# Performance work log

Measured on AMD Instinct MI355X. Metric: run time of the kernel, lower is better.

## Reference

```python
import jax, jax.numpy as jnp
import numpy as np


def _conv(x, w, b, stride, pad):
    y = jax.lax.conv_general_dilated(
        x, w, window_strides=(stride, stride),
        padding=((pad, pad), (pad, pad)),
        dimension_numbers=('NCHW', 'OIHW', 'NCHW'))
    return y + b[None, :, None, None]


def setup_inputs() -> dict:
    key = jax.random.key(0)
    ks = jax.random.split(key, 10)
    B, C, H, W = 4, 3, 256, 256
    HID, D, K = 128, 32, 65536
    s = 0.05
    return {
        'x': jax.random.normal(ks[0], (B, C, H, W), dtype=jnp.float32),
        'w1': jax.random.normal(ks[1], (HID, C, 4, 4), dtype=jnp.float32) * s,
        'b1': jnp.zeros((HID,), dtype=jnp.float32),
        'w2': jax.random.normal(ks[2], (HID, HID, 4, 4), dtype=jnp.float32) * s,
        'b2': jnp.zeros((HID,), dtype=jnp.float32),
        'w3': jax.random.normal(ks[3], (HID, HID, 4, 4), dtype=jnp.float32) * s,
        'b3': jnp.zeros((HID,), dtype=jnp.float32),
        'w4': jax.random.normal(ks[4], (D, HID, 3, 3), dtype=jnp.float32) * s,
        'b4': jnp.zeros((D,), dtype=jnp.float32),
        'codebook': jax.random.normal(ks[5], (K, D), dtype=jnp.float32),
    }


def reference(x, w1, b1, w2, b2, w3, b3, w4, b4, codebook):
    z = jax.nn.relu(_conv(x, w1, b1, 2, 1))
    z = jax.nn.relu(_conv(z, w2, b2, 2, 1))
    z = jax.nn.relu(_conv(z, w3, b3, 2, 1))
    z = _conv(z, w4, b4, 1, 1)                 # [B, D, h, w]
    z = jnp.transpose(z, (0, 2, 3, 1))          # [B, h, w, D]
    B, h, w, D = z.shape
    zf = z.reshape(-1, D)                        # [N, D]
    # pairwise squared distances: ||z||^2 + ||e||^2 - 2 z.e
    d = (jnp.sum(zf * zf, axis=1, keepdims=True)
         + jnp.sum(codebook * codebook, axis=1)[None, :]
         - 2.0 * jnp.matmul(zf, codebook.T))    # [N, K]
    idx = jnp.argmin(d, axis=1)                  # [N]
    z_q = codebook[idx].reshape(B, h, w, D)
    return idx.reshape(B, h, w), z_q
```

## Files before the change

### kernel.cpp

```cpp
#include <hip/hip_runtime.h>
#include <cfloat>

typedef float f32x4 __attribute__((ext_vector_type(4)));
typedef _Float16 h8 __attribute__((ext_vector_type(8)));

static __device__ __forceinline__ unsigned umin_(unsigned a, unsigned b) { return a < b ? a : b; }
static __device__ __forceinline__ unsigned umax_(unsigned a, unsigned b) { return a > b ? a : b; }
static __device__ __forceinline__ unsigned med3_(unsigned a, unsigned b, unsigned c) {
    unsigned d;
    asm("v_med3_u32 %0, %1, %2, %3" : "=v"(d) : "v"(a), "v"(b), "v"(c));
    return d;
}

static __device__ __forceinline__ void gl_lds16(const h8* g, h8* s) {
    __builtin_amdgcn_global_load_lds(
        (const __attribute__((address_space(1))) unsigned int*)g,
        (__attribute__((address_space(3))) unsigned int*)s, 16, 0, 0);
}

__global__ __launch_bounds__(256)
void prep_k(_Float16* p0, _Float16* p1, _Float16* p2, _Float16* p3,
            _Float16* p4, _Float16* p5,
            const float* __restrict__ w2, const float* __restrict__ w3,
            const float* __restrict__ w4,
            h8* __restrict__ B2h, h8* __restrict__ B2l,
            h8* __restrict__ B3h, h8* __restrict__ B3l,
            h8* __restrict__ B4h, h8* __restrict__ B4l) {
    const int bx = blockIdx.x;
    const int tid = threadIdx.x;

    if (bx < 96) {
        const int s = bx >> 4, plane = bx & 15;
        _Float16* p; int np, P;
        switch (s) {
            case 0: p = p0; np = 16; P = 66; break;
            case 1: p = p1; np = 16; P = 66; break;
            case 2: p = p2; np = 16; P = 34; break;
            case 3: p = p3; np = 16; P = 34; break;
            case 4: p = p4; np = 4;  P = 34; break;
            default: p = p5; np = 4; P = 34; break;
        }
        if (plane >= np) return;
        _Float16* pl = p + (size_t)plane * P * P * 128;
        const int rowN = P * 128;
        for (int i = tid; i < rowN; i += 256) {
            pl[i] = (_Float16)0.f;
            pl[(size_t)(P - 1) * rowN + i] = (_Float16)0.f;
            const int r = i >> 7, c = i & 127;
            pl[(size_t)r * rowN + c] = (_Float16)0.f;
            pl[(size_t)r * rowN + (P - 1) * 128 + c] = (_Float16)0.f;
        }
    } else {
        const int layer = (bx - 96) >> 7;
        const int bxx = (bx - 96) & 127;
        const float* w; h8 *Bh, *Bl; int T, NT, KHKW;
        switch (layer) {
            case 0:  w = w2; Bh = B2h; Bl = B2l; T = 16; NT = 8; KHKW = 16; break;
            case 1:  w = w3; Bh = B3h; Bl = B3l; T = 16; NT = 8; KHKW = 16; break;
            default: w = w4; Bh = B4h; Bl = B4l; T = 9;  NT = 2; KHKW = 9;  break;
        }
        const int idx = bxx * 256 + tid;
        if (idx >= T * 4 * NT * 64) return;
        const int lane = idx & 63;
        int r = idx >> 6;
        const int nt = r % NT; r /= NT;
        const int ks = r & 3;  r >>= 2;
        const int t = r;
        const int oc = nt * 16 + (lane & 15);
        const int icb = ks * 32 + (lane >> 4) * 8;
        h8 hv, lv;
#pragma unroll
        for (int j = 0; j < 8; ++j) {
            const float v = w[(size_t)(oc * 128 + icb + j) * KHKW + t];
            _Float16 h = (_Float16)v;
            hv[j] = h;
            lv[j] = (_Float16)((v - (float)h) * 2048.f);
        }
        Bh[idx] = hv;
        Bl[idx] = lv;
    }
}

__global__ __launch_bounds__(256)
void conv1_k(const float* __restrict__ in, const float* __restrict__ w,
             const float* __restrict__ bias,
             _Float16* __restrict__ Dh, _Float16* __restrict__ Dl) {
    __shared__ float tile[3][34 * 36];
    const int tid = threadIdx.x;
    const int tx = tid & 15, ty = tid >> 4;
    const int bx = blockIdx.x & 7, by = blockIdx.x >> 3;
    const int oc0 = blockIdx.y * 8;
    const int b = blockIdx.z;
    const int ox = bx * 16 + tx, oy = by * 16 + ty;
    const int ix0 = bx * 32 - 1, iy0 = by * 32 - 1;

    for (int f = tid; f < 3 * 34 * 34; f += 256) {
        const int ic = f / 1156, r2 = f % 1156;
        const int r = r2 / 34, c = r2 % 34;
        const int iy = iy0 + r, ix = ix0 + c;
        float v = ((unsigned)iy < 256u && (unsigned)ix < 256u)
                      ? in[((size_t)(b * 3 + ic) * 256 + iy) * 256 + ix] : 0.f;
        tile[ic][r * 36 + c] = v;
    }
    __syncthreads();

    float acc[8];
#pragma unroll
    for (int j = 0; j < 8; ++j) acc[j] = 0.f;
#pragma unroll
    for (int ic = 0; ic < 3; ++ic) {
#pragma unroll
        for (int kh = 0; kh < 4; ++kh) {
            const float2* p = (const float2*)&tile[ic][(2 * ty + kh) * 36 + 2 * tx];
            const float2 r0 = p[0], r1 = p[1];
            const float tap[4] = {r0.x, r0.y, r1.x, r1.y};
#pragma unroll
            for (int kw = 0; kw < 4; ++kw)
#pragma unroll
                for (int j = 0; j < 8; ++j)
                    acc[j] = fmaf(tap[kw], w[((oc0 + j) * 3 + ic) * 16 + kh * 4 + kw], acc[j]);
        }
    }

    h8 hv, lv;
#pragma unroll
    for (int j = 0; j < 8; ++j) {
        float r = fmaxf(acc[j] + bias[oc0 + j], 0.f);
        _Float16 h = (_Float16)r;
        hv[j] = h;
        lv[j] = (_Float16)((r - (float)h) * 2048.f);
    }
    const size_t di = (((size_t)((b * 2 + (oy & 1)) * 2 + (ox & 1)) * 66 + 1 + (oy >> 1)) * 66
                       + 1 + (ox >> 1)) * 128 + oc0;
    *(h8*)(Dh + di) = hv;
    *(h8*)(Dl + di) = lv;
}

template<int WN, int MT, bool SPLIT>
__global__ __launch_bounds__(256, 1)
void gemmS2_k(const _Float16* __restrict__ Ah, const _Float16* __restrict__ Al,
              const h8* __restrict__ Bh, const h8* __restrict__ Bl,
              const float* __restrict__ bias,
              _Float16* __restrict__ Dh, _Float16* __restrict__ Dl,
              int OW, int OH, int PP, int dPP) {
    constexpr int NW_N = 8 / WN;
    constexpr int NW_M = 4 / NW_N;
    __shared__ h8 lH[2][2048];
    __shared__ h8 lL[2][2048];

    const int tid = threadIdx.x, wid = tid >> 6, l = tid & 63;
    const int nq = wid % NW_N, mi = wid / NW_N;
    const int mt0 = (blockIdx.x * NW_M + mi) * MT;
    const int mpr = OW >> 4, mpi = OH * mpr;
    const int laneA = (l & 15) * 128 + (l >> 4) * 8;

    int bm[MT], oym[MT], oxm[MT];
#pragma unroll
    for (int m = 0; m < MT; ++m) {
        const int mt = mt0 + m;
        bm[m] = mt / mpi;
        const int rem = mt % mpi;
        oym[m] = rem / mpr;
        oxm[m] = (rem % mpr) << 4;
    }

    f32x4 a1[MT][WN], am[MT][WN];
#pragma unroll
    for (int m = 0; m < MT; ++m)
#pragma unroll
        for (int s = 0; s < WN; ++s) {
            a1[m][s] = (f32x4){0.f, 0.f, 0.f, 0.f};
            am[m][s] = (f32x4){0.f, 0.f, 0.f, 0.f};
        }

    {
        const h8* sh = Bh + wid * 512 + l;
        const h8* sl = Bl + wid * 512 + l;
#pragma unroll
        for (int i = 0; i < 8; ++i) gl_lds16(sh + i * 64, &lH[0][wid * 512 + i * 64]);
#pragma unroll
        for (int i = 0; i < 8; ++i) gl_lds16(sl + i * 64, &lL[0][wid * 512 + i * 64]);
    }
    __syncthreads();

#pragma unroll 1
    for (int t = 0; t < 16; ++t) {
        const int cur = t & 1;
        const int kh = t >> 2, kw = t & 3;
        const int dy = (kh - 1) >> 1, dx = (kw - 1) >> 1;
        const int py = (kh - 1) & 1, px = (kw - 1) & 1;
        h8 avh[MT][4], avl[MT][4];
#pragma unroll
        for (int m = 0; m < MT; ++m) {
            const int pidx = (bm[m] * 2 + py) * 2 + px;
            const size_t abase = ((size_t)(pidx * PP + (oym[m] + dy + 1)) * PP
                                  + (oxm[m] + dx + 1)) * 128 + laneA;
#pragma unroll
            for (int ks = 0; ks < 4; ++ks) {
                avh[m][ks] = *(const h8*)(Ah + abase + ks * 32);
                avl[m][ks] = *(const h8*)(Al + abase + ks * 32);
            }
        }
        if (t + 1 < 16) {
            const int nxt = cur ^ 1;
            const h8* sh = Bh + (size_t)(t + 1) * 2048 + wid * 512 + l;
            const h8* sl = Bl + (size_t)(t + 1) * 2048 + wid * 512 + l;
#pragma unroll
            for (int i = 0; i < 8; ++i) gl_lds16(sh + i * 64, &lH[nxt][wid * 512 + i * 64]);
#pragma unroll
            for (int i = 0; i < 8; ++i) gl_lds16(sl + i * 64, &lL[nxt][wid * 512 + i * 64]);
        }
#pragma unroll
        for (int ks = 0; ks < 4; ++ks) {
#pragma unroll
            for (int s = 0; s < WN; ++s) {
                const h8 bvh = lH[cur][(ks * 8 + nq * WN + s) * 64 + l];
                const h8 bvl = lL[cur][(ks * 8 + nq * WN + s) * 64 + l];
#pragma unroll
                for (int m = 0; m < MT; ++m) {
                    a1[m][s] = __builtin_amdgcn_mfma_f32_16x16x32_f16(avh[m][ks], bvh, a1[m][s], 0, 0, 0);
                    am[m][s] = __builtin_amdgcn_mfma_f32_16x16x32_f16(avh[m][ks], bvl, am[m][s], 0, 0, 0);
                    am[m][s] = __builtin_amdgcn_mfma_f32_16x16x32_f16(avl[m][ks], bvh, am[m][s], 0, 0, 0);
                }
            }
        }
        __syncthreads();
    }

#pragma unroll
    for (int m = 0; m < MT; ++m) {
#pragma unroll
        for (int s = 0; s < WN; ++s) {
            const int oc = (nq * WN + s) * 16 + (l & 15);
            const float bv = bias[oc];
#pragma unroll
            for (int i = 0; i < 4; ++i) {
                const int row = (l >> 4) * 4 + i;
                float v = fmaf(am[m][s][i], 4.8828125e-4f, a1[m][s][i]);
                v = fmaxf(v + bv, 0.f);
                _Float16 h = (_Float16)v;
                _Float16 lo = (_Float16)((v - (float)h) * 2048.f);
                const int oxp = oxm[m] + row;
                const int oy = oym[m], b = bm[m];
                size_t di;
                if constexpr (SPLIT) {
                    di = (((size_t)((b * 2 + (oy & 1)) * 2 + (oxp & 1)) * dPP
                           + 1 + (oy >> 1)) * dPP + 1 + (oxp >> 1)) * 128 + oc;
                } else {
                    di = ((size_t)(b * dPP + 1 + oy) * dPP + 1 + oxp) * 128 + oc;
                }
                Dh[di] = h;
                Dl[di] = lo;
            }
        }
    }
}

template<int S, bool FIN, int WPN, int MT>
__global__ __launch_bounds__(256)
void gemm_k(const _Float16* __restrict__ Ah, const _Float16* __restrict__ Al,
            const h8* __restrict__ Bh, const h8* __restrict__ Bl,
            float* __restrict__ part, const float* __restrict__ bias,
            _Float16* __restrict__ Dh, _Float16* __restrict__ Dl,
            int OW, int OH, int PP, int NT, int TPS, int M, int N, int dPP) {
    const int tid = threadIdx.x, wid = tid >> 6, l = tid & 63;
    const int ntb = wid % WPN;
    const int mt0 = (blockIdx.x * (4 / WPN) + wid / WPN) * MT;
    const int sp = blockIdx.y;
    const int mpr = OW >> 4, mpi = OH * mpr;
    const int laneA = (l & 15) * 128 + (l >> 4) * 8;

    int bmt[MT], oymt[MT], oxmt[MT];
#pragma unroll
    for (int m = 0; m < MT; ++m) {
        const int mt = mt0 + m;
        bmt[m] = mt / mpi;
        const int rem = mt % mpi;
        oymt[m] = rem / mpr;
        oxmt[m] = (rem % mpr) << 4;
    }

    f32x4 a1[MT][2], am[MT][2];
#pragma unroll
    for (int m = 0; m < MT; ++m)
#pragma unroll
        for (int s = 0; s < 2; ++s) {
            a1[m][s] = (f32x4){0.f, 0.f, 0.f, 0.f};
            am[m][s] = (f32x4){0.f, 0.f, 0.f, 0.f};
        }

    const int t0 = sp * TPS, t1 = t0 + TPS;
#pragma unroll 2
    for (int t = t0; t < t1; ++t) {
        int dy, dx, pidx[MT];
        if constexpr (S == 2) {
            const int kh = t >> 2, kw = t & 3;
            dy = (kh - 1) >> 1; dx = (kw - 1) >> 1;
            const int py = (kh - 1) & 1, px = (kw - 1) & 1;
#pragma unroll
            for (int m = 0; m < MT; ++m) pidx[m] = (bmt[m] * 2 + py) * 2 + px;
        } else {
            dy = t / 3 - 1; dx = t % 3 - 1;
#pragma unroll
            for (int m = 0; m < MT; ++m) pidx[m] = bmt[m];
        }
        const _Float16* pAh[MT]; const _Float16* pAl[MT];
#pragma unroll
        for (int m = 0; m < MT; ++m) {
            const size_t base = ((size_t)(pidx[m] * PP + (oymt[m] + dy + 1)) * PP
                                 + (oxmt[m] + dx + 1)) * 128 + laneA;
            pAh[m] = Ah + base;
            pAl[m] = Al + base;
        }
        const size_t bbase = ((size_t)(t * 4) * NT + ntb * 2) * 64 + l;
#pragma unroll
        for (int ks = 0; ks < 4; ++ks) {
            h8 avh[MT], avl[MT];
#pragma unroll
            for (int m = 0; m < MT; ++m) {
                avh[m] = *(const h8*)(pAh[m] + ks * 32);
                avl[m] = *(const h8*)(pAl[m] + ks * 32);
            }
#pragma unroll
            for (int s = 0; s < 2; ++s) {
                const h8 bvh = Bh[bbase + (size_t)ks * NT * 64 + s * 64];
                const h8 bvl = Bl[bbase + (size_t)ks * NT * 64 + s * 64];
#pragma unroll
                for (int m = 0; m < MT; ++m) {
                    a1[m][s] = __builtin_amdgcn_mfma_f32_16x16x32_f16(avh[m], bvh, a1[m][s], 0, 0, 0);
                    am[m][s] = __builtin_amdgcn_mfma_f32_16x16x32_f16(avh[m], bvl, am[m][s], 0, 0, 0);
                    am[m][s] = __builtin_amdgcn_mfma_f32_16x16x32_f16(avl[m], bvh, am[m][s], 0, 0, 0);
                }
            }
        }
    }

#pragma unroll
    for (int m = 0; m < MT; ++m) {
        const int mt = mt0 + m;
#pragma unroll
        for (int s = 0; s < 2; ++s) {
            const int oc = ntb * 32 + s * 16 + (l & 15);
#pragma unroll
            for (int i = 0; i < 4; ++i) {
                const int row = (l >> 4) * 4 + i;
                float v = fmaf(am[m][s][i], 4.8828125e-4f, a1[m][s][i]);
                if (!FIN) {
                    part[((size_t)sp * M + mt * 16 + row) * N + oc] = v;
                } else {
                    v = fmaxf(v + bias[oc], 0.f);
                    _Float16 h = (_Float16)v;
                    _Float16 lo = (_Float16)((v - (float)h) * 2048.f);
                    const int ox = oxmt[m] + row;
                    const int oy = oymt[m], b = bmt[m];
                    const size_t di = (((size_t)((b * 2 + (oy & 1)) * 2 + (ox & 1)) * dPP
                                        + 1 + (oy >> 1)) * dPP + 1 + (ox >> 1)) * 128 + oc;
                    Dh[di] = h;
                    Dl[di] = lo;
                }
            }
        }
    }
}

__global__ __launch_bounds__(256)
void fin4_k(const float* __restrict__ part, const float* __restrict__ bias,
            float* __restrict__ zz, h8* __restrict__ zh, h8* __restrict__ zl) {
    const int t = blockIdx.x * 256 + threadIdx.x;
    const int m = t >> 2, g8 = (t & 3) * 8;
    float v[8];
#pragma unroll
    for (int j = 0; j < 8; ++j) v[j] = bias[g8 + j];
#pragma unroll
    for (int sp = 0; sp < 3; ++sp) {
        const float4* p = (const float4*)(part + ((size_t)sp * 4096 + m) * 32 + g8);
        float4 x0 = p[0], x1 = p[1];
        v[0] += x0.x; v[1] += x0.y; v[2] += x0.z; v[3] += x0.w;
        v[4] += x1.x; v[5] += x1.y; v[6] += x1.z; v[7] += x1.w;
    }
    float4* dst = (float4*)(zz + (size_t)m * 32 + g8);
    dst[0] = make_float4(v[0], v[1], v[2], v[3]);
    dst[1] = make_float4(v[4], v[5], v[6], v[7]);
    h8 hv, lv;
#pragma unroll
    for (int j = 0; j < 8; ++j) {
        const float mv = -2.f * v[j];
        _Float16 h = (_Float16)mv;
        hv[j] = h;
        lv[j] = (_Float16)(mv - (float)h);
    }
    const int idx = (m >> 4) * 64 + (m & 15) + (t & 3) * 16;
    zh[idx] = hv;
    zl[idx] = lv;
}

#define VQ_NSPLIT 64
#define VQ_KSPC   1024
#define VQ_NCHUNK 8
#define VQ_TAU_S  102.4f
#define VQ_ABS_S  524288.0f
#define VQ_QT     4

__global__ __launch_bounds__(256)
void split_cb_k(const float* __restrict__ cb, h8* __restrict__ cbh, h8* __restrict__ cbl,
                float* __restrict__ cbn2, float* __restrict__ cbn_raw,
                unsigned* __restrict__ counter) {
    const int c = blockIdx.x * 256 + threadIdx.x;
    const float4* p = (const float4*)(cb + (size_t)c * 32);
    float e[32];
    float s = 0.f;
#pragma unroll
    for (int i = 0; i < 8; ++i) {
        float4 v = p[i];
        e[i*4+0] = v.x; e[i*4+1] = v.y; e[i*4+2] = v.z; e[i*4+3] = v.w;
        s += v.x*v.x + v.y*v.y + v.z*v.z + v.w*v.w;
    }
    cbn_raw[c] = s;
    cbn2[c]    = (s + 512.0f) * 2048.0f;
    const int base = (c >> 4) * 64 + (c & 15);
#pragma unroll
    for (int g = 0; g < 4; ++g) {
        h8 hv, lv;
#pragma unroll
        for (int j = 0; j < 8; ++j) {
            float v = e[g*8 + j];
            _Float16 h = (_Float16)v;
            hv[j] = (_Float16)((float)h * 2048.0f);
            lv[j] = (_Float16)((v - (float)h) * 2048.0f);
        }
        cbh[base + g*16] = hv;
        cbl[base + g*16] = lv;
    }
    if (c == 0) *counter = 0u;
}

__global__ __launch_bounds__(256, 4)
void vq_mfma_k(const h8* __restrict__ zh, const h8* __restrict__ zl,
               const uint4* __restrict__ cbh, const uint4* __restrict__ cbl,
               const float* __restrict__ cbn2,
               unsigned* __restrict__ pb1, unsigned* __restrict__ pb2,
               unsigned* __restrict__ pcol) {
    __shared__ uint4 lH[2][512];
    __shared__ uint4 lL[2][512];
    __shared__ float lN[2][128];

    const int tid = threadIdx.x;
    const int w = tid >> 6, ln = tid & 63;
    const int split = blockIdx.y;
    const int qt0 = (blockIdx.x * 4 + w) * VQ_QT;

    h8 azh[VQ_QT], azl[VQ_QT];
#pragma unroll
    for (int qq = 0; qq < VQ_QT; ++qq) {
        azh[qq] = zh[(qt0 + qq) * 64 + ln];
        azl[qq] = zl[(qt0 + qq) * 64 + ln];
    }

    unsigned b1[VQ_QT][4], b2[VQ_QT][4];
#pragma unroll
    for (int qq = 0; qq < VQ_QT; ++qq)
#pragma unroll
        for (int i = 0; i < 4; ++i) { b1[qq][i] = 0x7F800000u; b2[qq][i] = 0x7F800000u; }

    const int fbase = split * (VQ_KSPC * 4);
    const int nbase = split * VQ_KSPC;

    {
        uint4 h0 = cbh[fbase + tid], h1 = cbh[fbase + 256 + tid];
        uint4 l0 = cbl[fbase + tid], l1 = cbl[fbase + 256 + tid];
        lH[0][tid] = h0; lH[0][tid + 256] = h1;
        lL[0][tid] = l0; lL[0][tid + 256] = l1;
        if (tid < 128) lN[0][tid] = cbn2[nbase + tid];
    }
    __syncthreads();

    for (int ci = 0; ci < VQ_NCHUNK; ++ci) {
        const int cur = ci & 1;
        const bool more = (ci + 1 < VQ_NCHUNK);
        uint4 nh0, nh1, nl0, nl1; float nn = 0.f;
        if (more) {
            const int nb = fbase + (ci + 1) * 512;
            nh0 = cbh[nb + tid]; nh1 = cbh[nb + 256 + tid];
            nl0 = cbl[nb + tid]; nl1 = cbl[nb + 256 + tid];
            if (tid < 128) nn = cbn2[nbase + (ci + 1) * 128 + tid];
        }

        const unsigned tcb = (unsigned)(ci * 8);
#pragma unroll
        for (int t = 0; t < 8; ++t) {
            const h8 bh = *reinterpret_cast<const h8*>(&lH[cur][t*64 + ln]);
            const h8 bl = *reinterpret_cast<const h8*>(&lL[cur][t*64 + ln]);
            const float nv = lN[cur][t*16 + (ln & 15)];
            f32x4 nvv = {nv, nv, nv, nv};
            const unsigned tc = tcb + t;
#pragma unroll
            for (int qq = 0; qq < VQ_QT; ++qq) {
                f32x4 acc;
                acc = __builtin_amdgcn_mfma_f32_16x16x32_f16(azh[qq], bh, nvv, 0, 0, 0);
                acc = __builtin_amdgcn_mfma_f32_16x16x32_f16(azh[qq], bl, acc, 0, 0, 0);
                acc = __builtin_amdgcn_mfma_f32_16x16x32_f16(azl[qq], bh, acc, 0, 0, 0);
#pragma unroll
                for (int i = 0; i < 4; ++i) {
                    const unsigned k0 = (__float_as_uint(acc[i]) & 0xFFFFFF00u) | tc;
                    b2[qq][i] = med3_(b1[qq][i], b2[qq][i], k0);
                    b1[qq][i] = umin_(b1[qq][i], k0);
                }
            }
        }

        if (more) {
            const int nxt = cur ^ 1;
            lH[nxt][tid] = nh0; lH[nxt][tid + 256] = nh1;
            lL[nxt][tid] = nl0; lL[nxt][tid + 256] = nl1;
            if (tid < 128) lN[nxt][tid] = nn;
        }
        __syncthreads();
    }

#pragma unroll
    for (int qq = 0; qq < VQ_QT; ++qq) {
#pragma unroll
        for (int i = 0; i < 4; ++i) {
            unsigned v1 = b1[qq][i], v2 = b2[qq][i], cv = (unsigned)(ln & 15);
#pragma unroll
            for (int m = 1; m < 16; m <<= 1) {
                unsigned o1 = __shfl_xor(v1, m, 64);
                unsigned o2 = __shfl_xor(v2, m, 64);
                unsigned oc = __shfl_xor(cv, m, 64);
                unsigned nb2 = umin_(umin_(v2, o2), umax_(v1, o1));
                if (o1 < v1) cv = oc;
                v1 = umin_(v1, o1); v2 = nb2;
            }
            if ((ln & 15) == 0) {
                const int q = (qt0 + qq) * 16 + (ln >> 4) * 4 + i;
                pb1[(size_t)q * VQ_NSPLIT + split] = v1;
                pb2[(size_t)q * VQ_NSPLIT + split] = v2;
                pcol[(size_t)q * VQ_NSPLIT + split] = cv;
            }
        }
    }
}

__global__ __launch_bounds__(256)
void combine_k(const unsigned* __restrict__ pb1, const unsigned* __restrict__ pb2,
               const unsigned* __restrict__ pcol,
               unsigned* __restrict__ coarse, unsigned* __restrict__ flags,
               unsigned* __restrict__ list, unsigned* __restrict__ counter) {
    const int q = blockIdx.x * 256 + threadIdx.x;
    unsigned B1 = 0x7F800000u, B2 = 0x7F800000u, PAY = 0u;
#pragma unroll 4
    for (int s = 0; s < VQ_NSPLIT; ++s) {
        unsigned a1 = pb1[(size_t)q * VQ_NSPLIT + s];
        unsigned a2 = pb2[(size_t)q * VQ_NSPLIT + s];
        unsigned ac = pcol[(size_t)q * VQ_NSPLIT + s];
        unsigned nb2 = umin_(umin_(B2, a2), umax_(B1, a1));
        if (a1 < B1) PAY = ((unsigned)s << 4) | ac;
        B1 = umin_(B1, a1); B2 = nb2;
    }
    const unsigned tile = B1 & 0xFFu;
    const unsigned code = (PAY >> 4) * VQ_KSPC + tile * 16 + (PAY & 15u);
    const float f1 = __uint_as_float(B1 & 0xFFFFFF00u);
    const float f2 = __uint_as_float(B2 & 0xFFFFFF00u);
    const int fl = (f2 - f1 < VQ_TAU_S) || (f1 < VQ_ABS_S);
    coarse[q] = code;
    flags[q] = (unsigned)fl;
    if (fl) { unsigned p = atomicAdd(counter, 1u); list[p] = q; }
}

__global__ __launch_bounds__(256)
void guard_k(const float* __restrict__ cb, const float* __restrict__ cbn_raw,
             const float* __restrict__ zz, const unsigned* __restrict__ list,
             const unsigned* __restrict__ counter, float2* __restrict__ gpart) {
    __shared__ float lcb[256 * 36];
    __shared__ float lnr[256];
    __shared__ int ns;

    const int tid = threadIdx.x;
    const int w = tid >> 6, ln = tid & 63;
    const int bx = blockIdx.x;

    const float4* cb4 = (const float4*)cb;
#pragma unroll
    for (int it = 0; it < 8; ++it) {
        const int f = tid + it * 256;
        float4 v = cb4[(size_t)bx * 2048 + f];
        const int c = f >> 3, g = f & 7;
        *(float4*)&lcb[c * 36 + g * 4] = v;
    }
    lnr[tid] = cbn_raw[bx * 256 + tid];
    if (tid == 0) ns = (int)*(volatile unsigned*)counter;
    __syncthreads();

    for (int ii = blockIdx.y * 4 + w; ii < ns; ii += 32) {
        const int q = (int)list[ii];
        const float4* zq = (const float4*)(zz + (size_t)q * 32);
        float m2[32];
#pragma unroll
        for (int j = 0; j < 8; ++j) {
            float4 v = zq[j];
            m2[j*4+0] = -2.f*v.x; m2[j*4+1] = -2.f*v.y; m2[j*4+2] = -2.f*v.z; m2[j*4+3] = -2.f*v.w;
        }
        float bv = FLT_MAX; int bc = 0x7FFFFFFF;
#pragma unroll
        for (int cc = 0; cc < 4; ++cc) {
            const int c = cc * 64 + ln;
            float d = lnr[c];
#pragma unroll
            for (int j = 0; j < 8; ++j) {
                float4 e = *(const float4*)&lcb[c * 36 + j * 4];
                d = fmaf(m2[j*4+0], e.x, d);
                d = fmaf(m2[j*4+1], e.y, d);
                d = fmaf(m2[j*4+2], e.z, d);
                d = fmaf(m2[j*4+3], e.w, d);
            }
            if (d < bv || (d == bv && c < bc)) { bv = d; bc = c; }
        }
#pragma unroll
        for (int m = 1; m < 64; m <<= 1) {
            float ov = __shfl_xor(bv, m, 64);
            int   oi = __shfl_xor(bc, m, 64);
            if (ov < bv || (ov == bv && oi < bc)) { bv = ov; bc = oi; }
        }
        if (ln == 0) gpart[(size_t)q * 256 + bx] = make_float2(bv, (float)(bx * 256 + bc));
    }
}

__global__ __launch_bounds__(256)
void final_k(const unsigned* __restrict__ flags, const unsigned* __restrict__ coarse,
             const float2* __restrict__ gpart, const float* __restrict__ cb,
             float* __restrict__ out_idx, float* __restrict__ out_zq) {
    const int tid = threadIdx.x, w = tid >> 6, ln = tid & 63;
    const int q = blockIdx.x * 4 + w;
    int bi;
    if (flags[q]) {
        float bv = FLT_MAX; int bidx = 0x7FFFFFFF;
#pragma unroll
        for (int k = 0; k < 4; ++k) {
            const int b = k * 64 + ln;
            float2 o = gpart[(size_t)q * 256 + b];
            int oi = (int)o.y;
            if (o.x < bv || (o.x == bv && oi < bidx)) { bv = o.x; bidx = oi; }
        }
#pragma unroll
        for (int m = 1; m < 64; m <<= 1) {
            float ov = __shfl_xor(bv, m, 64);
            int   oi = __shfl_xor(bidx, m, 64);
            if (ov < bv || (ov == bv && oi < bidx)) { bv = ov; bidx = oi; }
        }
        bi = bidx;
    } else {
        bi = (int)coarse[q];
    }
    if (ln == 0) out_idx[q] = (float)bi;
    if (ln < 8) {
        float4 v = ((const float4*)(cb + (size_t)bi * 32))[ln];
        ((float4*)(out_zq + (size_t)q * 32))[ln] = v;
    }
}

extern "C" void kernel_launch(void* const* d_in, const int* in_sizes, int n_in,
                              void* d_out, int out_size, void* d_ws, size_t ws_size,
                              hipStream_t stream) {
    const float* x  = (const float*)d_in[0];
    const float* w1 = (const float*)d_in[1];
    const float* b1 = (const float*)d_in[2];
    const float* w2 = (const float*)d_in[3];
    const float* b2 = (const float*)d_in[4];
    const float* w3 = (const float*)d_in[5];
    const float* b3 = (const float*)d_in[6];
    const float* w4 = (const float*)d_in[7];
    const float* b4 = (const float*)d_in[8];
    const float* cb = (const float*)d_in[9];
    float* out = (float*)d_out;

    float* ws = (float*)d_ws;
    _Float16* y1h = (_Float16*)ws;
    _Float16* y1l = (_Float16*)(ws + 4460544);
    _Float16* y2h = (_Float16*)(ws + 8921088);
    _Float16* y2l = (_Float16*)(ws + 10104832);
    _Float16* y3h = (_Float16*)(ws + 11288576);
    _Float16* y3l = (_Float16*)(ws + 11584512);
    float* zzp = ws + 11880448;
    h8* B2h = (h8*)(ws + 12011520);
    h8* B2l = (h8*)(ws + 12142592);
    h8* B3h = (h8*)(ws + 12273664);
    h8* B3l = (h8*)(ws + 12404736);
    h8* B4h = (h8*)(ws + 12535808);
    h8* B4l = (h8*)(ws + 12554240);
    float* part = ws + 12572672;
    h8*       cbh     = (h8*)ws;
    h8*       cbl     = (h8*)(ws + 1048576);
    h8*       zh      = (h8*)(ws + 2097152);
    h8*       zl      = (h8*)(ws + 2162688);
    float*    cbn2    = ws + 2228224;
    float*    cbn_raw = ws + 2293760;
    unsigned* pb1     = (unsigned*)(ws + 2359296);
    unsigned* pb2     = (unsigned*)(ws + 2621440);
    unsigned* pcol    = (unsigned*)(ws + 2883584);
    unsigned* coarse  = (unsigned*)(ws + 3145728);
    unsigned* flags   = (unsigned*)(ws + 3149824);
    unsigned* list    = (unsigned*)(ws + 3153920);
    unsigned* counter = (unsigned*)(ws + 3158016);
    float2*   gpart   = (float2*)(ws + 3158080);

    prep_k<<<480, 256, 0, stream>>>(y1h, y1l, y2h, y2l, y3h, y3l,
                                    w2, w3, w4, B2h, B2l, B3h, B3l, B4h, B4l);
    conv1_k<<<dim3(64, 16, 4), 256, 0, stream>>>(x, w1, b1, y1h, y1l);
    gemmS2_k<4, 2, true><<<dim3(256), 256, 0, stream>>>(y1h, y1l, B2h, B2l, b2, y2h, y2l,
                                                        64, 64, 66, 34);
    gemmS2_k<2, 1, false><<<dim3(256), 256, 0, stream>>>(y2h, y2l, B3h, B3l, b3, y3h, y3l,
                                                         32, 32, 34, 34);
    gemm_k<1, false, 1, 1><<<dim3(64, 3), 256, 0, stream>>>(y3h, y3l, B4h, B4l, part, nullptr, nullptr, nullptr,
                                                            32, 32, 34, 2, 3, 4096, 32, 0);
    fin4_k<<<64, 256, 0, stream>>>(part, b4, zzp, zh, zl);

    split_cb_k<<<256, 256, 0, stream>>>(cb, cbh, cbl, cbn2, cbn_raw, counter);
    vq_mfma_k <<<dim3(16, VQ_NSPLIT), 256, 0, stream>>>(zh, zl, (const uint4*)cbh, (const uint4*)cbl,
                                                        cbn2, pb1, pb2, pcol);
    combine_k <<<16,  256, 0, stream>>>(pb1, pb2, pcol, coarse, flags, list, counter);
    guard_k   <<<dim3(256, 8), 256, 0, stream>>>(cb, cbn_raw, zzp, list, counter, gpart);
    final_k   <<<1024, 256, 0, stream>>>(flags, coarse, gpart, cb, out, out + 4096);
}
```

Baseline: 237.5 us.

## Fuse final 3x3 conv epilogue and codebook split into one kernel

Replaces the split-K gemm for the last 3x3 projection, its separate partial-sum reduction kernel, and the codebook preprocessing kernel with a single launch. The first 128 blocks compute the full K reduction per tile and apply bias and the fp16 hi/lo split directly. The remaining blocks perform the codebook split and norms. This removes two launches and the partial-sum round trip through memory. In exchange, the conv path loses split-K parallelism and writes scalar fp16 elements instead of vector stores.

```diff
diff --git a/kernel.cpp b/kernel.cpp
--- a/kernel.cpp
+++ b/kernel.cpp
@@ -256,142 +256,90 @@
     }
 }
 
-template<int S, bool FIN, int WPN, int MT>
 __global__ __launch_bounds__(256)
-void gemm_k(const _Float16* __restrict__ Ah, const _Float16* __restrict__ Al,
-            const h8* __restrict__ Bh, const h8* __restrict__ Bl,
-            float* __restrict__ part, const float* __restrict__ bias,
-            _Float16* __restrict__ Dh, _Float16* __restrict__ Dl,
-            int OW, int OH, int PP, int NT, int TPS, int M, int N, int dPP) {
-    const int tid = threadIdx.x, wid = tid >> 6, l = tid & 63;
-    const int ntb = wid % WPN;
-    const int mt0 = (blockIdx.x * (4 / WPN) + wid / WPN) * MT;
-    const int sp = blockIdx.y;
-    const int mpr = OW >> 4, mpi = OH * mpr;
-    const int laneA = (l & 15) * 128 + (l >> 4) * 8;
-
-    int bmt[MT], oymt[MT], oxmt[MT];
-#pragma unroll
-    for (int m = 0; m < MT; ++m) {
-        const int mt = mt0 + m;
-        bmt[m] = mt / mpi;
+void conv4f_k(const _Float16* __restrict__ Ah, const _Float16* __restrict__ Al,
+              const h8* __restrict__ Bh, const h8* __restrict__ Bl,
+              const float* __restrict__ bias,
+              float* __restrict__ zz, _Float16* __restrict__ zh, _Float16* __restrict__ zl,
+              const float* __restrict__ cb, h8* __restrict__ cbh, h8* __restrict__ cbl,
+              float* __restrict__ cbn2, float* __restrict__ cbn_raw,
+              unsigned* __restrict__ counter) {
+    const int bx = blockIdx.x;
+    const int tid = threadIdx.x;
+
+    if (bx < 128) {
+        const int wid = tid >> 6, l = tid & 63;
+        const int nq = wid & 1, mi = wid >> 1;
+        const int mt = bx * 2 + mi;
+        const int mpr = 2, mpi = 64;
+        const int b = mt / mpi;
         const int rem = mt % mpi;
-        oymt[m] = rem / mpr;
-        oxmt[m] = (rem % mpr) << 4;
-    }
-
-    f32x4 a1[MT][2], am[MT][2];
-#pragma unroll
-    for (int m = 0; m < MT; ++m)
-#pragma unroll
-        for (int s = 0; s < 2; ++s) {
-            a1[m][s] = (f32x4){0.f, 0.f, 0.f, 0.f};
-            am[m][s] = (f32x4){0.f, 0.f, 0.f, 0.f};
-        }
-
-    const int t0 = sp * TPS, t1 = t0 + TPS;
-#pragma unroll 2
-    for (int t = t0; t < t1; ++t) {
-        int dy, dx, pidx[MT];
-        if constexpr (S == 2) {
-            const int kh = t >> 2, kw = t & 3;
-            dy = (kh - 1) >> 1; dx = (kw - 1) >> 1;
-            const int py = (kh - 1) & 1, px = (kw - 1) & 1;
-#pragma unroll
-            for (int m = 0; m < MT; ++m) pidx[m] = (bmt[m] * 2 + py) * 2 + px;
-        } else {
-            dy = t / 3 - 1; dx = t % 3 - 1;
-#pragma unroll
-            for (int m = 0; m < MT; ++m) pidx[m] = bmt[m];
-        }
-        const _Float16* pAh[MT]; const _Float16* pAl[MT];
-#pragma unroll
-        for (int m = 0; m < MT; ++m) {
-            const size_t base = ((size_t)(pidx[m] * PP + (oymt[m] + dy + 1)) * PP
-                                 + (oxmt[m] + dx + 1)) * 128 + laneA;
-            pAh[m] = Ah + base;
-            pAl[m] = Al + base;
-        }
-        const size_t bbase = ((size_t)(t * 4) * NT + ntb * 2) * 64 + l;
-#pragma unroll
-        for (int ks = 0; ks < 4; ++ks) {
-            h8 avh[MT], avl[MT];
-#pragma unroll
-            for (int m = 0; m < MT; ++m) {
-                avh[m] = *(const h8*)(pAh[m] + ks * 32);
-                avl[m] = *(const h8*)(pAl[m] + ks * 32);
-            }
-#pragma unroll
-            for (int s = 0; s < 2; ++s) {
-                const h8 bvh = Bh[bbase + (size_t)ks * NT * 64 + s * 64];
-                const h8 bvl = Bl[bbase + (size_t)ks * NT * 64 + s * 64];
-#pragma unroll
-                for (int m = 0; m < MT; ++m) {
-                    a1[m][s] = __builtin_amdgcn_mfma_f32_16x16x32_f16(avh[m], bvh, a1[m][s], 0, 0, 0);
-                    am[m][s] = __builtin_amdgcn_mfma_f32_16x16x32_f16(avh[m], bvl, am[m][s], 0, 0, 0);
-                    am[m][s] = __builtin_amdgcn_mfma_f32_16x16x32_f16(avl[m], bvh, am[m][s], 0, 0, 0);
-                }
-            }
-        }
-    }
-
-#pragma unroll
-    for (int m = 0; m < MT; ++m) {
-        const int mt = mt0 + m;
-#pragma unroll
-        for (int s = 0; s < 2; ++s) {
-            const int oc = ntb * 32 + s * 16 + (l & 15);
-#pragma unroll
-            for (int i = 0; i < 4; ++i) {
-                const int row = (l >> 4) * 4 + i;
-                float v = fmaf(am[m][s][i], 4.8828125e-4f, a1[m][s][i]);
-                if (!FIN) {
-                    part[((size_t)sp * M + mt * 16 + row) * N + oc] = v;
-                } else {
-                    v = fmaxf(v + bias[oc], 0.f);
-                    _Float16 h = (_Float16)v;
-                    _Float16 lo = (_Float16)((v - (float)h) * 2048.f);
-                    const int ox = oxmt[m] + row;
-                    const int oy = oymt[m], b = bmt[m];
-                    const size_t di = (((size_t)((b * 2 + (oy & 1)) * 2 + (ox & 1)) * dPP
-                                        + 1 + (oy >> 1)) * dPP + 1 + (ox >> 1)) * 128 + oc;
-                    Dh[di] = h;
-                    Dl[di] = lo;
-                }
-            }
-        }
-    }
-}
-
-__global__ __launch_bounds__(256)
-void fin4_k(const float* __restrict__ part, const float* __restrict__ bias,
-            float* __restrict__ zz, h8* __restrict__ zh, h8* __restrict__ zl) {
-    const int t = blockIdx.x * 256 + threadIdx.x;
-    const int m = t >> 2, g8 = (t & 3) * 8;
-    float v[8];
-#pragma unroll
-    for (int j = 0; j < 8; ++j) v[j] = bias[g8 + j];
-#pragma unroll
-    for (int sp = 0; sp < 3; ++sp) {
-        const float4* p = (const float4*)(part + ((size_t)sp * 4096 + m) * 32 + g8);
-        float4 x0 = p[0], x1 = p[1];
-        v[0] += x0.x; v[1] += x0.y; v[2] += x0.z; v[3] += x0.w;
-        v[4] += x1.x; v[5] += x1.y; v[6] += x1.z; v[7] += x1.w;
-    }
-    float4* dst = (float4*)(zz + (size_t)m * 32 + g8);
-    dst[0] = make_float4(v[0], v[1], v[2], v[3]);
-    dst[1] = make_float4(v[4], v[5], v[6], v[7]);
-    h8 hv, lv;
-#pragma unroll
-    for (int j = 0; j < 8; ++j) {
-        const float mv = -2.f * v[j];
-        _Float16 h = (_Float16)mv;
-        hv[j] = h;
-        lv[j] = (_Float16)(mv - (float)h);
-    }
-    const int idx = (m >> 4) * 64 + (m & 15) + (t & 3) * 16;
-    zh[idx] = hv;
-    zl[idx] = lv;
+        const int oy = rem / mpr, ox = (rem % mpr) << 4;
+        const int laneA = (l & 15) * 128 + (l >> 4) * 8;
+
+        f32x4 a1 = {0.f, 0.f, 0.f, 0.f}, am = {0.f, 0.f, 0.f, 0.f};
+
+#pragma unroll 1
+        for (int t = 0; t < 9; ++t) {
+            const int dy = t / 3 - 1, dx = t % 3 - 1;
+            const size_t abase = ((size_t)(b * 34 + (oy + dy + 1)) * 34
+                                  + (ox + dx + 1)) * 128 + laneA;
+#pragma unroll
+            for (int ks = 0; ks < 4; ++ks) {
+                const h8 avh = *(const h8*)(Ah + abase + ks * 32);
+                const h8 avl = *(const h8*)(Al + abase + ks * 32);
+                const h8 bvh = Bh[((size_t)(t * 4 + ks) * 2 + nq) * 64 + l];
+                const h8 bvl = Bl[((size_t)(t * 4 + ks) * 2 + nq) * 64 + l];
+                a1 = __builtin_amdgcn_mfma_f32_16x16x32_f16(avh, bvh, a1, 0, 0, 0);
+                am = __builtin_amdgcn_mfma_f32_16x16x32_f16(avh, bvl, am, 0, 0, 0);
+                am = __builtin_amdgcn_mfma_f32_16x16x32_f16(avl, bvh, am, 0, 0, 0);
+            }
+        }
+
+        const int oc = nq * 16 + (l & 15);
+        const float bv = bias[oc];
+#pragma unroll
+        for (int i = 0; i < 4; ++i) {
+            const int row = (l >> 4) * 4 + i;
+            const int q = mt * 16 + row;
+            const float v = fmaf(am[i], 4.8828125e-4f, a1[i]) + bv;
+            zz[(size_t)q * 32 + oc] = v;
+            const float mv = -2.f * v;
+            _Float16 hh = (_Float16)mv;
+            _Float16 ll = (_Float16)(mv - (float)hh);
+            const size_t zi = ((size_t)(q >> 4) * 64 + (q & 15) + ((oc >> 3) << 4)) * 8 + (oc & 7);
+            zh[zi] = hh;
+            zl[zi] = ll;
+        }
+    } else {
+        const int c = (bx - 128) * 256 + tid;
+        const float4* p = (const float4*)(cb + (size_t)c * 32);
+        float e[32];
+        float s = 0.f;
+#pragma unroll
+        for (int i = 0; i < 8; ++i) {
+            float4 v = p[i];
+            e[i*4+0] = v.x; e[i*4+1] = v.y; e[i*4+2] = v.z; e[i*4+3] = v.w;
+            s += v.x*v.x + v.y*v.y + v.z*v.z + v.w*v.w;
+        }
+        cbn_raw[c] = s;
+        cbn2[c]    = (s + 512.0f) * 2048.0f;
+        const int base = (c >> 4) * 64 + (c & 15);
+#pragma unroll
+        for (int g = 0; g < 4; ++g) {
+            h8 hv, lv;
+#pragma unroll
+            for (int j = 0; j < 8; ++j) {
+                float v = e[g*8 + j];
+                _Float16 h = (_Float16)v;
+                hv[j] = (_Float16)((float)h * 2048.0f);
+                lv[j] = (_Float16)((v - (float)h) * 2048.0f);
+            }
+            cbh[base + g*16] = hv;
+            cbl[base + g*16] = lv;
+        }
+        if (c == 0) *counter = 0u;
+    }
 }
 
 #define VQ_NSPLIT 64
@@ -400,39 +348,6 @@
 #define VQ_TAU_S  102.4f
 #define VQ_ABS_S  524288.0f
 #define VQ_QT     4
-
-__global__ __launch_bounds__(256)
-void split_cb_k(const float* __restrict__ cb, h8* __restrict__ cbh, h8* __restrict__ cbl,
-                float* __restrict__ cbn2, float* __restrict__ cbn_raw,
-                unsigned* __restrict__ counter) {
-    const int c = blockIdx.x * 256 + threadIdx.x;
-    const float4* p = (const float4*)(cb + (size_t)c * 32);
-    float e[32];
-    float s = 0.f;
-#pragma unroll
-    for (int i = 0; i < 8; ++i) {
-        float4 v = p[i];
-        e[i*4+0] = v.x; e[i*4+1] = v.y; e[i*4+2] = v.z; e[i*4+3] = v.w;
-        s += v.x*v.x + v.y*v.y + v.z*v.z + v.w*v.w;
-    }
-    cbn_raw[c] = s;
-    cbn2[c]    = (s + 512.0f) * 2048.0f;
-    const int base = (c >> 4) * 64 + (c & 15);
-#pragma unroll
-    for (int g = 0; g < 4; ++g) {
-        h8 hv, lv;
-#pragma unroll
-        for (int j = 0; j < 8; ++j) {
-            float v = e[g*8 + j];
-            _Float16 h = (_Float16)v;
-            hv[j] = (_Float16)((float)h * 2048.0f);
-            lv[j] = (_Float16)((v - (float)h) * 2048.0f);
-        }
-        cbh[base + g*16] = hv;
-        cbl[base + g*16] = lv;
-    }
-    if (c == 0) *counter = 0u;
-}
 
 __global__ __launch_bounds__(256, 4)
 void vq_mfma_k(const h8* __restrict__ zh, const h8* __restrict__ zl,
@@ -688,6 +603,7 @@
     h8* B4h = (h8*)(ws + 12535808);
     h8* B4l = (h8*)(ws + 12554240);
     float* part = ws + 12572672;
+    (void)part;
     h8*       cbh     = (h8*)ws;
     h8*       cbl     = (h8*)(ws + 1048576);
     h8*       zh      = (h8*)(ws + 2097152);
@@ -710,11 +626,10 @@
                                                         64, 64, 66, 34);
     gemmS2_k<2, 1, false><<<dim3(256), 256, 0, stream>>>(y2h, y2l, B3h, B3l, b3, y3h, y3l,
                                                          32, 32, 34, 34);
-    gemm_k<1, false, 1, 1><<<dim3(64, 3), 256, 0, stream>>>(y3h, y3l, B4h, B4l, part, nullptr, nullptr, nullptr,
-                                                            32, 32, 34, 2, 3, 4096, 32, 0);
-    fin4_k<<<64, 256, 0, stream>>>(part, b4, zzp, zh, zl);
-
-    split_cb_k<<<256, 256, 0, stream>>>(cb, cbh, cbl, cbn2, cbn_raw, counter);
+    conv4f_k<<<384, 256, 0, stream>>>(y3h, y3l, B4h, B4l, b4,
+                                      zzp, (_Float16*)zh, (_Float16*)zl,
+                                      cb, cbh, cbl, cbn2, cbn_raw, counter);
+
     vq_mfma_k <<<dim3(16, VQ_NSPLIT), 256, 0, stream>>>(zh, zl, (const uint4*)cbh, (const uint4*)cbl,
                                                         cbn2, pb1, pb2, pcol);
     combine_k <<<16,  256, 0, stream>>>(pb1, pb2, pcol, coarse, flags, list, counter);
```

Measured after the change: 239.5 us. About the same (+0.8%).
